# Performance work log

Measured on AMD Instinct MI355X. Metric: run time of the kernel, lower is better.

The kernel has to match this reference:

```python
import jax, jax.numpy as jnp
import numpy as np

DICT_SIZE = 512
EMBED_DIM = 64
SPARSITY = 5
COMMITMENT_COST = 0.25
EPSILON = 1e-10
COEFF_CLAMP = 1e7


def setup_inputs() -> dict:
    key = jax.random.key(0)
    kz, kd = jax.random.split(key)
    z = jax.random.normal(kz, (32, EMBED_DIM, 32, 32), dtype=jnp.float32)
    D = jax.random.normal(kd, (EMBED_DIM, DICT_SIZE), dtype=jnp.float32)
    # _normalize_dictionary(): unit L2 norm per atom (column)
    D = D / jnp.linalg.norm(D, axis=0, keepdims=True)
    return {"z": z, "dictionary": D}


def batch_omp(signals, dictionary):
    # signals: [E, N], dictionary: [E, K]
    E, N = signals.shape
    K = dictionary.shape[1]
    Dt = dictionary.T  # [K, E]
    DtD = Dt @ dictionary + EPSILON * jnp.eye(K, dtype=signals.dtype)  # [K, K]
    residual = signals
    active = jnp.zeros((N, K), dtype=bool)
    coefficients = jnp.zeros((N, K), dtype=signals.dtype)
    idx = jnp.zeros((N, 0), dtype=jnp.int32)
    rows = jnp.arange(N)
    for k in range(SPARSITY):  # small fixed unroll; active-set size is static k+1
        corr = Dt @ residual                                  # [K, N]
        corr = jnp.where(active.T, -jnp.inf, corr)
        new_atoms = jnp.argmax(corr, axis=0).astype(jnp.int32)  # [N]
        active = active.at[rows, new_atoms].set(True)
        idx = jnp.concatenate([idx, new_atoms[:, None]], axis=1)  # [N, k+1]
        G = DtD[idx[:, :, None], idx[:, None, :]]             # [N, k+1, k+1]
        y = jnp.einsum('nke,en->nk', Dt[idx], residual)       # [N, k+1]
        coeffs = jnp.linalg.solve(G, y[..., None])[..., 0]    # [N, k+1]
        update = jnp.einsum('enk,nk->en', dictionary[:, idx], coeffs)  # [E, N]
        residual = signals - update
        coefficients = coefficients.at[rows[:, None], idx].set(coeffs)
    return coefficients.T  # [K, N]


def reference(z, dictionary):
    B, E, H, W = z.shape
    # [B,E,H,W] -> [E, N]
    z_flat = z.transpose(0, 2, 3, 1).reshape(-1, E).T
    # sparse coding is done under no_grad in torch
    coefficients = jax.lax.stop_gradient(batch_omp(z_flat, dictionary))
    coefficients = jnp.clip(coefficients, -COEFF_CLAMP, COEFF_CLAMP)  # [K, N]
    z_q_flat = dictionary @ coefficients                               # [E, N]
    z_q_reshaped = z_q_flat.T.reshape(B, H, W, E).transpose(0, 3, 1, 2)
    rec_loss = jnp.mean((jax.lax.stop_gradient(z_q_flat) - z_flat) ** 2)
    commit_loss = jnp.mean((z_q_flat - jax.lax.stop_gradient(z_flat)) ** 2)
    effective_cost = COMMITMENT_COST * (1.0 + SPARSITY / 10.0)
    coeff_loss = jnp.mean(jnp.abs(coefficients))
    loss = rec_loss + effective_cost * commit_loss + 0.001 * coeff_loss
    # straight-through estimator with clamp
    z_q = z + jax.lax.stop_gradient(jnp.clip(z_q_reshaped - z, -1.0, 1.0))
    return z_q, loss, coefficients
```

## Files before the change

kernel.cpp:

```cpp
#include <hip/hip_runtime.h>
#include <math.h>

#define NSIG 32768
#define KD   512
#define ED   64
#define SP   5

__host__ __device__ constexpr int TRI(int i, int j) {
  return i * SP - i * (i + 1) / 2 + j;
}

__global__ __launch_bounds__(256) void k_dtd(const float* __restrict__ D,
                                             double* __restrict__ DtD) {
  int flat = blockIdx.x * 256 + threadIdx.x;
  int i = flat >> 9, j = flat & 511;
  double acc = 0.0;
  #pragma unroll
  for (int e = 0; e < ED; ++e)
    acc += (double)D[e * KD + i] * (double)D[e * KD + j];
  if (i == j) acc += 1e-10;
  DtD[flat] = acc;
}

__global__ __launch_bounds__(256) void k_zero(float* __restrict__ p, size_t count) {
  size_t i = (size_t)blockIdx.x * 256 + threadIdx.x;
  size_t stride = (size_t)gridDim.x * 256;
  for (; i < count; i += stride) p[i] = 0.0f;
}

__global__ __launch_bounds__(256) void k_corr0(const float* __restrict__ z,
                                               const float* __restrict__ D,
                                               double* __restrict__ corr0, int n0) {
  int tid = threadIdx.x;
  int g  = tid & 63;
  int sg = tid >> 6;
  int srel = blockIdx.x * 16 + sg * 4;
  int n = n0 + srel;
  int b = n >> 10, p = n & 1023;
  const float* zp = z + (size_t)b * 65536 + p;
  const float* dp = D + g * 8;
  double acc[4][8];
  #pragma unroll
  for (int s = 0; s < 4; ++s)
    #pragma unroll
    for (int a = 0; a < 8; ++a) acc[s][a] = 0.0;
  for (int e = 0; e < ED; ++e) {
    const float4 zv = *(const float4*)(zp + (size_t)e * 1024);
    const float4 d0 = *(const float4*)(dp + (size_t)e * KD);
    const float4 d1 = *(const float4*)(dp + (size_t)e * KD + 4);
    double dz[4] = {(double)zv.x, (double)zv.y, (double)zv.z, (double)zv.w};
    double dd[8] = {(double)d0.x, (double)d0.y, (double)d0.z, (double)d0.w,
                    (double)d1.x, (double)d1.y, (double)d1.z, (double)d1.w};
    #pragma unroll
    for (int s = 0; s < 4; ++s)
      #pragma unroll
      for (int a = 0; a < 8; ++a) acc[s][a] += dz[s] * dd[a];
  }
  #pragma unroll
  for (int s = 0; s < 4; ++s) {
    double* o = corr0 + (size_t)(srel + s) * KD + g * 8;
    #pragma unroll
    for (int a = 0; a < 8; ++a) o[a] = acc[s][a];
  }
}

template <int K>
__device__ __forceinline__ void omp_iter(const double* __restrict__ c0row,
                                         const double* __restrict__ DtD,
                                         const double (&c0)[16], unsigned& amask,
                                         int (&idx)[SP], double (&cc)[SP],
                                         double (&tri)[15], double (&c0sel)[SP],
                                         int li) {
  double vb = -INFINITY;
  int ab = 0x7FFFFFFF;
  #pragma unroll
  for (int j = 0; j < 16; ++j) {
    int a = (j << 5) + li;
    double v = c0[j];
    #pragma unroll
    for (int m = 0; m < K; ++m)
      v -= DtD[(size_t)idx[m] * KD + a] * cc[m];
    v = ((amask >> j) & 1u) ? -INFINITY : v;
    if (v > vb) { vb = v; ab = a; }
  }
  #pragma unroll
  for (int s = 16; s >= 1; s >>= 1) {
    double ov = __shfl_xor(vb, s, 64);
    int    oa = __shfl_xor(ab, s, 64);
    if (ov > vb || (ov == vb && oa < ab)) { vb = ov; ab = oa; }
  }
  idx[K] = ab;
  if ((ab & 31) == li) amask |= 1u << (ab >> 5);
  c0sel[K] = c0row[ab];
  const double* drow = DtD + (size_t)ab * KD;
  double b[SP], u[SP];
  #pragma unroll
  for (int m = 0; m < K; ++m) b[m] = drow[idx[m]];
  double sch = drow[ab];
  #pragma unroll
  for (int i = 0; i < K; ++i) {
    double ui = 0.0;
    #pragma unroll
    for (int m = 0; m < K; ++m) {
      int lo = i < m ? i : m, hi = i < m ? m : i;
      ui += tri[lo * SP - lo * (lo + 1) / 2 + hi] * b[m];
    }
    u[i] = ui;
    sch -= b[i] * ui;
  }
  double r = 1.0 / sch;
  #pragma unroll
  for (int i = 0; i < K; ++i) {
    #pragma unroll
    for (int j = i; j < K; ++j) tri[i * SP - i * (i + 1) / 2 + j] += r * u[i] * u[j];
    tri[i * SP - i * (i + 1) / 2 + K] = -r * u[i];
  }
  tri[K * SP - K * (K + 1) / 2 + K] = r;
  double h[SP];
  #pragma unroll
  for (int i = 0; i <= K; ++i) {
    double s = 0.0;
    #pragma unroll
    for (int j = 0; j <= K; ++j) {
      int lo = i < j ? i : j, hi = i < j ? j : i;
      s += tri[lo * SP - lo * (lo + 1) / 2 + hi] * c0sel[j];
    }
    h[i] = s;
  }
  #pragma unroll
  for (int i = 0; i < K; ++i) cc[i] = h[i] - cc[i];
  cc[K] = h[K];
}

__global__ __launch_bounds__(256) void k_omp(const double* __restrict__ corr0,
                                             const double* __restrict__ DtD,
                                             float* __restrict__ coefOut,
                                             int* __restrict__ idxWs,
                                             double* __restrict__ cWs,
                                             double* __restrict__ csumWs, int n0) {
  int tid = threadIdx.x;
  int lane = tid & 63;
  int li = lane & 31;
  int g  = lane >> 5;
  int sigRel = blockIdx.x * 8 + (tid >> 6) * 2 + g;
  int n = n0 + sigRel;
  const double* c0row = corr0 + (size_t)sigRel * KD;
  double c0[16];
  #pragma unroll
  for (int j = 0; j < 16; ++j) c0[j] = c0row[(j << 5) + li];
  unsigned amask = 0;
  int idx[SP]; double cc[SP]; double tri[15]; double c0sel[SP];
  omp_iter<0>(c0row, DtD, c0, amask, idx, cc, tri, c0sel, li);
  omp_iter<1>(c0row, DtD, c0, amask, idx, cc, tri, c0sel, li);
  omp_iter<2>(c0row, DtD, c0, amask, idx, cc, tri, c0sel, li);
  omp_iter<3>(c0row, DtD, c0, amask, idx, cc, tri, c0sel, li);
  omp_iter<4>(c0row, DtD, c0, amask, idx, cc, tri, c0sel, li);
  if (li == 0) {
    double cs = 0.0;
    #pragma unroll
    for (int j = 0; j < SP; ++j) {
      double cj = cc[j];
      cj = fmin(fmax(cj, -10000000.0), 10000000.0);
      cs += fabs(cj);
      idxWs[n * SP + j] = idx[j];
      cWs[n * SP + j] = cj;
      coefOut[(size_t)idx[j] * NSIG + n] = (float)cj;
    }
    csumWs[n] = cs;
  }
}

__global__ __launch_bounds__(256) void k_zq(const float* __restrict__ z,
                                            const float* __restrict__ D,
                                            const int* __restrict__ idxWs,
                                            const double* __restrict__ cWs,
                                            float* __restrict__ zqOut,
                                            double* __restrict__ recWs) {
  int t = threadIdx.x;
  size_t flat = (size_t)blockIdx.x * 256 + t;
  int b = (int)(flat >> 16);
  int e = (int)((flat >> 10) & 63);
  int p = (int)(flat & 1023);
  int n = b * 1024 + p;
  double u = 0.0;
  #pragma unroll
  for (int j = 0; j < SP; ++j) {
    int a = idxWs[n * SP + j];
    u += (double)D[e * KD + a] * cWs[n * SP + j];
  }
  float zv = z[flat];
  double d = u - (double)zv;
  double dc = fmin(fmax(d, -1.0), 1.0);
  zqOut[flat] = (float)((double)zv + dc);
  __shared__ double red[256];
  red[t] = d * d;
  __syncthreads();
  #pragma unroll
  for (int s = 128; s >= 1; s >>= 1) {
    if (t < s) red[t] += red[t + s];
    __syncthreads();
  }
  if (t == 0) recWs[blockIdx.x] = red[0];
}

__global__ __launch_bounds__(256) void k_loss(const double* __restrict__ recWs,
                                              const double* __restrict__ csumWs,
                                              float* __restrict__ lossOut) {
  int t = threadIdx.x;
  double r = 0.0, c = 0.0;
  for (int i = t; i < 8192; i += 256) r += recWs[i];
  for (int i = t; i < NSIG; i += 256) c += csumWs[i];
  __shared__ double red[512];
  red[t] = r; red[256 + t] = c;
  __syncthreads();
  #pragma unroll
  for (int s = 128; s >= 1; s >>= 1) {
    if (t < s) { red[t] += red[t + s]; red[256 + t] += red[256 + t + s]; }
    __syncthreads();
  }
  if (t == 0) {
    double rec = red[0] / (double)(64.0 * 32768.0);
    double cm  = red[256] / (double)(512.0 * 32768.0);
    double loss = rec + 0.375 * rec + 0.001 * cm;
    lossOut[0] = (float)loss;
  }
}

extern "C" void kernel_launch(void* const* d_in, const int* in_sizes, int n_in,
                              void* d_out, int out_size, void* d_ws, size_t ws_size,
                              hipStream_t stream) {
  const float* z = (const float*)d_in[0];
  const float* D = (const float*)d_in[1];
  float* out = (float*)d_out;
  float* zqOut   = out;
  float* lossOut = out + 2097152;
  float* coefOut = out + 2097153;

  char* w = (char*)d_ws;
  double* DtD    = (double*)w; w += (size_t)KD * KD * 8;
  int*    idxWs  = (int*)w;    w += (size_t)NSIG * SP * 4;
  double* cWs    = (double*)w; w += (size_t)NSIG * SP * 8;
  double* csumWs = (double*)w; w += (size_t)NSIG * 8;
  double* recWs  = (double*)w; w += (size_t)8192 * 8;
  double* corr0  = (double*)w;
  size_t fixed = (size_t)(w - (char*)d_ws);
  long long avail = (long long)ws_size - (long long)fixed;
  int chunk = NSIG;
  while (chunk > 1024 && (long long)chunk * KD * 8 > avail) chunk >>= 1;

  k_dtd<<<1024, 256, 0, stream>>>(D, DtD);
  k_zero<<<4096, 256, 0, stream>>>(coefOut, (size_t)KD * NSIG);
  for (int n0 = 0; n0 < NSIG; n0 += chunk) {
    int cs = NSIG - n0; if (cs > chunk) cs = chunk;
    k_corr0<<<cs / 16, 256, 0, stream>>>(z, D, corr0, n0);
    k_omp<<<cs / 8, 256, 0, stream>>>(corr0, DtD, coefOut, idxWs, cWs, csumWs, n0);
  }
  k_zq<<<8192, 256, 0, stream>>>(z, D, idxWs, cWs, zqOut, recWs);
  k_loss<<<1, 256, 0, stream>>>(recWs, csumWs, lossOut);
}
```

Measured before the change: 247.4 us.

## Fuse initial correlation into OMP kernel via LDS-staged dictionary tiles

Removes the separate corr0 kernel and its 128MB double workspace round-trip. Each OMP block now computes its signals' initial correlations itself, staging 16-row dictionary tiles in shared memory, and the per-lane atom mapping becomes paired columns so DtD rows can be read as double2. The selected atom's initial correlation is rebuilt from the running max plus the DtD terms instead of reloaded from memory. In exchange every block reloads the full dictionary into LDS (128KB of global reads per 8 signals), and the 32KB of shared memory per block may reduce occupancy.

```diff
diff --git a/kernel.cpp b/kernel.cpp
--- a/kernel.cpp
+++ b/kernel.cpp
@@ -5,10 +5,6 @@
 #define KD   512
 #define ED   64
 #define SP   5
-
-__host__ __device__ constexpr int TRI(int i, int j) {
-  return i * SP - i * (i + 1) / 2 + j;
-}
 
 __global__ __launch_bounds__(256) void k_dtd(const float* __restrict__ D,
                                              double* __restrict__ DtD) {
@@ -28,45 +24,8 @@
   for (; i < count; i += stride) p[i] = 0.0f;
 }
 
-__global__ __launch_bounds__(256) void k_corr0(const float* __restrict__ z,
-                                               const float* __restrict__ D,
-                                               double* __restrict__ corr0, int n0) {
-  int tid = threadIdx.x;
-  int g  = tid & 63;
-  int sg = tid >> 6;
-  int srel = blockIdx.x * 16 + sg * 4;
-  int n = n0 + srel;
-  int b = n >> 10, p = n & 1023;
-  const float* zp = z + (size_t)b * 65536 + p;
-  const float* dp = D + g * 8;
-  double acc[4][8];
-  #pragma unroll
-  for (int s = 0; s < 4; ++s)
-    #pragma unroll
-    for (int a = 0; a < 8; ++a) acc[s][a] = 0.0;
-  for (int e = 0; e < ED; ++e) {
-    const float4 zv = *(const float4*)(zp + (size_t)e * 1024);
-    const float4 d0 = *(const float4*)(dp + (size_t)e * KD);
-    const float4 d1 = *(const float4*)(dp + (size_t)e * KD + 4);
-    double dz[4] = {(double)zv.x, (double)zv.y, (double)zv.z, (double)zv.w};
-    double dd[8] = {(double)d0.x, (double)d0.y, (double)d0.z, (double)d0.w,
-                    (double)d1.x, (double)d1.y, (double)d1.z, (double)d1.w};
-    #pragma unroll
-    for (int s = 0; s < 4; ++s)
-      #pragma unroll
-      for (int a = 0; a < 8; ++a) acc[s][a] += dz[s] * dd[a];
-  }
-  #pragma unroll
-  for (int s = 0; s < 4; ++s) {
-    double* o = corr0 + (size_t)(srel + s) * KD + g * 8;
-    #pragma unroll
-    for (int a = 0; a < 8; ++a) o[a] = acc[s][a];
-  }
-}
-
 template <int K>
-__device__ __forceinline__ void omp_iter(const double* __restrict__ c0row,
-                                         const double* __restrict__ DtD,
+__device__ __forceinline__ void omp_iter(const double* __restrict__ DtD,
                                          const double (&c0)[16], unsigned& amask,
                                          int (&idx)[SP], double (&cc)[SP],
                                          double (&tri)[15], double (&c0sel)[SP],
@@ -74,14 +33,19 @@
   double vb = -INFINITY;
   int ab = 0x7FFFFFFF;
   #pragma unroll
-  for (int j = 0; j < 16; ++j) {
-    int a = (j << 5) + li;
-    double v = c0[j];
-    #pragma unroll
-    for (int m = 0; m < K; ++m)
-      v -= DtD[(size_t)idx[m] * KD + a] * cc[m];
-    v = ((amask >> j) & 1u) ? -INFINITY : v;
-    if (v > vb) { vb = v; ab = a; }
+  for (int j2 = 0; j2 < 8; ++j2) {
+    int a0 = (j2 << 6) + (li << 1);
+    double v0 = c0[2 * j2], v1 = c0[2 * j2 + 1];
+    #pragma unroll
+    for (int m = 0; m < K; ++m) {
+      double2 g2 = *(const double2*)(DtD + (size_t)idx[m] * KD + a0);
+      v0 -= g2.x * cc[m];
+      v1 -= g2.y * cc[m];
+    }
+    v0 = ((amask >> (2 * j2)) & 1u) ? -INFINITY : v0;
+    v1 = ((amask >> (2 * j2 + 1)) & 1u) ? -INFINITY : v1;
+    if (v0 > vb) { vb = v0; ab = a0; }
+    if (v1 > vb) { vb = v1; ab = a0 + 1; }
   }
   #pragma unroll
   for (int s = 16; s >= 1; s >>= 1) {
@@ -90,12 +54,17 @@
     if (ov > vb || (ov == vb && oa < ab)) { vb = ov; ab = oa; }
   }
   idx[K] = ab;
-  if ((ab & 31) == li) amask |= 1u << (ab >> 5);
-  c0sel[K] = c0row[ab];
+  if (((ab >> 1) & 31) == li) amask |= 1u << ((((ab >> 6) << 1)) | (ab & 1));
   const double* drow = DtD + (size_t)ab * KD;
-  double b[SP], u[SP];
-  #pragma unroll
-  for (int m = 0; m < K; ++m) b[m] = drow[idx[m]];
+  double bb[SP], u[SP];
+  #pragma unroll
+  for (int m = 0; m < K; ++m) bb[m] = drow[idx[m]];
+  {
+    double csel = vb;
+    #pragma unroll
+    for (int m = 0; m < K; ++m) csel += bb[m] * cc[m];
+    c0sel[K] = csel;
+  }
   double sch = drow[ab];
   #pragma unroll
   for (int i = 0; i < K; ++i) {
@@ -103,10 +72,10 @@
     #pragma unroll
     for (int m = 0; m < K; ++m) {
       int lo = i < m ? i : m, hi = i < m ? m : i;
-      ui += tri[lo * SP - lo * (lo + 1) / 2 + hi] * b[m];
+      ui += tri[lo * SP - lo * (lo + 1) / 2 + hi] * bb[m];
     }
     u[i] = ui;
-    sch -= b[i] * ui;
+    sch -= bb[i] * ui;
   }
   double r = 1.0 / sch;
   #pragma unroll
@@ -132,29 +101,59 @@
   cc[K] = h[K];
 }
 
-__global__ __launch_bounds__(256) void k_omp(const double* __restrict__ corr0,
-                                             const double* __restrict__ DtD,
-                                             float* __restrict__ coefOut,
-                                             int* __restrict__ idxWs,
-                                             double* __restrict__ cWs,
-                                             double* __restrict__ csumWs, int n0) {
+__global__ __launch_bounds__(256) void k_fused(const float* __restrict__ z,
+                                               const float* __restrict__ D,
+                                               const double* __restrict__ DtD,
+                                               float* __restrict__ coefOut,
+                                               int* __restrict__ idxWs,
+                                               double* __restrict__ cWs,
+                                               double* __restrict__ csumWs) {
+  __shared__ float Dlds[16 * 512];
+  __shared__ float zbuf[64 * 8];
   int tid = threadIdx.x;
-  int lane = tid & 63;
-  int li = lane & 31;
-  int g  = lane >> 5;
-  int sigRel = blockIdx.x * 8 + (tid >> 6) * 2 + g;
-  int n = n0 + sigRel;
-  const double* c0row = corr0 + (size_t)sigRel * KD;
+  int li = tid & 31;
+  int mysig = ((tid >> 6) << 1) | ((tid >> 5) & 1);
+  int n = blockIdx.x * 8 + mysig;
+  int b = n >> 10, p0 = (blockIdx.x * 8) & 1023;
+  {
+    const float* zb = z + (size_t)b * 65536 + p0;
+    #pragma unroll
+    for (int k2 = 0; k2 < 2; ++k2) {
+      int f = tid + 256 * k2;
+      zbuf[f] = zb[(f >> 3) * 1024 + (f & 7)];
+    }
+  }
   double c0[16];
   #pragma unroll
-  for (int j = 0; j < 16; ++j) c0[j] = c0row[(j << 5) + li];
+  for (int j = 0; j < 16; ++j) c0[j] = 0.0;
+  for (int t4 = 0; t4 < 4; ++t4) {
+    __syncthreads();
+    {
+      const float4* src = (const float4*)(D + t4 * 16 * 512);
+      float4* dst = (float4*)Dlds;
+      #pragma unroll
+      for (int i = 0; i < 8; ++i) dst[tid + 256 * i] = src[tid + 256 * i];
+    }
+    __syncthreads();
+    #pragma unroll 4
+    for (int e = 0; e < 16; ++e) {
+      double zv = (double)zbuf[(t4 * 16 + e) * 8 + mysig];
+      const float* drow = Dlds + e * 512;
+      #pragma unroll
+      for (int j2 = 0; j2 < 8; ++j2) {
+        float2 dv = *(const float2*)(drow + (j2 << 6) + (li << 1));
+        c0[2 * j2]     += zv * (double)dv.x;
+        c0[2 * j2 + 1] += zv * (double)dv.y;
+      }
+    }
+  }
   unsigned amask = 0;
   int idx[SP]; double cc[SP]; double tri[15]; double c0sel[SP];
-  omp_iter<0>(c0row, DtD, c0, amask, idx, cc, tri, c0sel, li);
-  omp_iter<1>(c0row, DtD, c0, amask, idx, cc, tri, c0sel, li);
-  omp_iter<2>(c0row, DtD, c0, amask, idx, cc, tri, c0sel, li);
-  omp_iter<3>(c0row, DtD, c0, amask, idx, cc, tri, c0sel, li);
-  omp_iter<4>(c0row, DtD, c0, amask, idx, cc, tri, c0sel, li);
+  omp_iter<0>(DtD, c0, amask, idx, cc, tri, c0sel, li);
+  omp_iter<1>(DtD, c0, amask, idx, cc, tri, c0sel, li);
+  omp_iter<2>(DtD, c0, amask, idx, cc, tri, c0sel, li);
+  omp_iter<3>(DtD, c0, amask, idx, cc, tri, c0sel, li);
+  omp_iter<4>(DtD, c0, amask, idx, cc, tri, c0sel, li);
   if (li == 0) {
     double cs = 0.0;
     #pragma unroll
@@ -242,19 +241,10 @@
   double* cWs    = (double*)w; w += (size_t)NSIG * SP * 8;
   double* csumWs = (double*)w; w += (size_t)NSIG * 8;
   double* recWs  = (double*)w; w += (size_t)8192 * 8;
-  double* corr0  = (double*)w;
-  size_t fixed = (size_t)(w - (char*)d_ws);
-  long long avail = (long long)ws_size - (long long)fixed;
-  int chunk = NSIG;
-  while (chunk > 1024 && (long long)chunk * KD * 8 > avail) chunk >>= 1;
 
   k_dtd<<<1024, 256, 0, stream>>>(D, DtD);
   k_zero<<<4096, 256, 0, stream>>>(coefOut, (size_t)KD * NSIG);
-  for (int n0 = 0; n0 < NSIG; n0 += chunk) {
-    int cs = NSIG - n0; if (cs > chunk) cs = chunk;
-    k_corr0<<<cs / 16, 256, 0, stream>>>(z, D, corr0, n0);
-    k_omp<<<cs / 8, 256, 0, stream>>>(corr0, DtD, coefOut, idxWs, cWs, csumWs, n0);
-  }
+  k_fused<<<NSIG / 8, 256, 0, stream>>>(z, D, DtD, coefOut, idxWs, cWs, csumWs);
   k_zq<<<8192, 256, 0, stream>>>(z, D, idxWs, cWs, zqOut, recWs);
   k_loss<<<1, 256, 0, stream>>>(recWs, csumWs, lossOut);
 }
```

Result: faster. 233.8 us (-5.5%).
